# Kernel tuning notes

Measured on AMD Instinct MI355X. Metric: run time of the kernel, lower is better.

## Reference

```python
import jax, jax.numpy as jnp
import numpy as np

EPS = 1e-5
H = 8  # num_heads

def _bn(x, g, b):
    # training-mode BatchNorm over the LAST axis as channels; stats over all other axes
    axes = tuple(range(x.ndim - 1))
    mean = jnp.mean(x, axis=axes)
    var = jnp.var(x, axis=axes)  # biased, matches torch BN normalization
    return (x - mean) * jax.lax.rsqrt(var + EPS) * g + b


def setup_inputs() -> dict:
    key = jax.random.key(0)
    ks = jax.random.split(key, 16)
    m, S, C = 256, 128, 256
    s = 1.0 / np.sqrt(C)
    inp = {
        'x': jax.random.normal(ks[0], (m, S, C), jnp.float32),
        'g_n': jnp.ones((C,), jnp.float32), 'b_n': jnp.zeros((C,), jnp.float32),
        'Wq': jax.random.normal(ks[1], (C, C), jnp.float32) * s,
        'Wk': jax.random.normal(ks[2], (C, C), jnp.float32) * s,
        'Wv': jax.random.normal(ks[3], (C, C), jnp.float32) * s,
        'Wo': jax.random.normal(ks[4], (C, C), jnp.float32) * s,
        'bo': jnp.zeros((C,), jnp.float32),
        'g_pe': jnp.ones((S * S,), jnp.float32), 'b_pe': jnp.zeros((S * S,), jnp.float32),
        'g0': jnp.ones((C,), jnp.float32), 'b0': jnp.zeros((C,), jnp.float32),
        'W0': jax.random.normal(ks[5], (2 * C, C), jnp.float32) * s,
        'g1': jnp.ones((2 * C,), jnp.float32), 'b1': jnp.zeros((2 * C,), jnp.float32),
        'W1': jax.random.normal(ks[6], (C, 2 * C), jnp.float32) * (1.0 / np.sqrt(2 * C)),
    }
    return inp


def reference(x, g_n, b_n, Wq, Wk, Wv, Wo, bo, g_pe, b_pe, g0, b0, W0, g1, b1, W1):
    m, S, C = x.shape
    d = C // H
    # --- SelfAttention ---
    h = _bn(x, g_n, b_n)  # BN over channels C, stats over (batch, seq)
    q = (h @ Wq.T).reshape(m, S, H, d)
    k = (h @ Wk.T).reshape(m, S, H, d)
    v = (h @ Wv.T).reshape(m, S, H, d)
    energy = jnp.einsum('nqhc,nkhc->nhqk', q, k)  # [m,H,S,S]
    # BatchNorm1d over the flattened S*S 'channel' axis, stats over (batch, heads)
    e = energy.reshape(m, H, S * S)
    e = _bn(e, g_pe, b_pe)
    energy_post = e.reshape(m, H, S, S)
    attn = jax.nn.softmax(energy_post / jnp.sqrt(jnp.float32(C)), axis=-1)
    o = jnp.einsum('nhql,nlhc->nqhc', attn, v).reshape(m, S, C)
    x1 = o @ Wo.T + bo + x  # residual
    # --- FFN block ---
    out0 = _bn(x1, g0, b0)
    out1 = jax.nn.relu(out0)
    out2 = out1 @ W0.T            # [m,S,2C]
    out3 = _bn(out2, g1, b1)
    out4 = jax.nn.relu(out3)
    out5 = out4 @ W1.T            # [m,S,C]
    return x1 + out5  # dropout p=0.0 -> identity
```

## Files before the change

kernel.cpp:

```cpp
#include <hip/hip_runtime.h>
#include <hip/hip_bf16.h>

#define HH 8
#define SS 128
#define CC 256
#define DD 32
#define NTOK 32768
#define NHB 2048
#define BNEPS 1e-5f

using bf16 = __hip_bfloat16;
typedef float f32x4 __attribute__((ext_vector_type(4)));
typedef __bf16 bf16x8 __attribute__((ext_vector_type(8)));

__device__ __forceinline__ bf16x8 ld8(const bf16* p) {
    return *reinterpret_cast<const bf16x8*>(p);
}
__device__ __forceinline__ f32x4 ldf4(const float* p) {
    return *reinterpret_cast<const f32x4*>(p);
}
__device__ __forceinline__ void st8(bf16* p, bf16x8 v) {
    *reinterpret_cast<bf16x8*>(p) = v;
}
__device__ __forceinline__ bf16 bfc(__bf16 x) {
    union { __bf16 i; bf16 o; } u;
    u.i = x;
    return u.o;
}
__device__ __forceinline__ int swzg(int row, int g) {
    return ((g & 8) | ((g & 7) ^ (row & 7))) << 3;
}

typedef __attribute__((address_space(1))) const void g_void;
typedef __attribute__((address_space(3))) void l_void;
__device__ __forceinline__ void gload_lds16(const bf16* g, bf16* l) {
    __builtin_amdgcn_global_load_lds((g_void*)g, (l_void*)l, 16, 0, 0);
}

__global__ __launch_bounds__(256) void prep(const float* __restrict__ wq,
                                            const float* __restrict__ wk,
                                            const float* __restrict__ wv,
                                            const float* __restrict__ wo,
                                            const float* __restrict__ w0,
                                            const float* __restrict__ w1,
                                            bf16* __restrict__ out,
                                            const float* __restrict__ X,
                                            float* __restrict__ part) {
    int tid = threadIdx.x;
    if (blockIdx.x < 512) {
        int i = (blockIdx.x * 256 + tid) * 4;
        const float* src;
        int off;
        if (i < 65536) { src = wq; off = i; }
        else if (i < 131072) { src = wk; off = i - 65536; }
        else if (i < 196608) { src = wv; off = i - 131072; }
        else if (i < 262144) { src = wo; off = i - 196608; }
        else if (i < 393216) { src = w0; off = i - 262144; }
        else { src = w1; off = i - 393216; }
        f32x4 v = ldf4(src + off);
#pragma unroll
        for (int u = 0; u < 4; u++) out[i + u] = __float2bfloat16(v[u]);
        return;
    }
    int bx = blockIdx.x - 512;
    int cv = tid & 63, slot = tid >> 6;
    int c0 = cv * 4;
    size_t row0 = (size_t)bx * 256 + slot;
    float s[4], s2[4];
#pragma unroll
    for (int u = 0; u < 4; u++) { s[u] = 0.f; s2[u] = 0.f; }
    for (int i = 0; i < 64; i++) {
        size_t row = row0 + (size_t)i * 4;
        f32x4 v = ldf4(X + row * 256 + c0);
#pragma unroll
        for (int u = 0; u < 4; u++) {
            float f = v[u];
            s[u] += f; s2[u] += f * f;
        }
    }
    __shared__ float red[256][8];
#pragma unroll
    for (int u = 0; u < 4; u++) {
        red[tid][u] = s[u];
        red[tid][4 + u] = s2[u];
    }
    __syncthreads();
    if (tid < 64) {
#pragma unroll
        for (int sl = 1; sl < 4; sl++)
#pragma unroll
            for (int u = 0; u < 4; u++) {
                s[u] += red[tid + sl * 64][u];
                s2[u] += red[tid + sl * 64][4 + u];
            }
        float* dst = part + (size_t)bx * 512;
#pragma unroll
        for (int u = 0; u < 4; u++) {
            dst[c0 + u] = s[u];
            dst[256 + c0 + u] = s2[u];
        }
    }
}

template <int CH, int P, int ROWS>
__global__ __launch_bounds__(256) void statsA_wide(const bf16* __restrict__ X,
                                                   float* __restrict__ part) {
    constexpr int RB = ROWS / P;
    int c0 = (blockIdx.x * 256 + threadIdx.x) * 8;
    size_t row0 = (size_t)blockIdx.y * RB;
    float s[8], s2[8];
#pragma unroll
    for (int u = 0; u < 8; u++) { s[u] = 0.f; s2[u] = 0.f; }
    for (int i = 0; i < RB; i++) {
        bf16x8 v = ld8(X + (row0 + i) * CH + c0);
#pragma unroll
        for (int u = 0; u < 8; u++) {
            float f = (float)v[u];
            s[u] += f; s2[u] += f * f;
        }
    }
    float* dst = part + (size_t)blockIdx.y * (2 * CH);
#pragma unroll
    for (int u = 0; u < 8; u++) {
        dst[c0 + u] = s[u];
        dst[CH + c0 + u] = s2[u];
    }
}

__global__ __launch_bounds__(256) void statsB(const float* __restrict__ part, int P,
                                              int nch, float inv_n, float ps,
                                              const float* __restrict__ gamma,
                                              const float* __restrict__ beta,
                                              float* __restrict__ scale,
                                              float* __restrict__ bias) {
    int cl = threadIdx.x & 63, sl = threadIdx.x >> 6;
    int c = blockIdx.x * 64 + cl;
    float s = 0.f, s2 = 0.f;
    for (int p = sl; p < P; p += 4) {
        s += part[(size_t)p * 2 * nch + c];
        s2 += part[(size_t)p * 2 * nch + nch + c];
    }
    __shared__ float red[2][4][64];
    red[0][sl][cl] = s;
    red[1][sl][cl] = s2;
    __syncthreads();
    if (threadIdx.x < 64) {
        s = red[0][0][cl] + red[0][1][cl] + red[0][2][cl] + red[0][3][cl];
        s2 = red[1][0][cl] + red[1][1][cl] + red[1][2][cl] + red[1][3][cl];
        float mean = s * inv_n;
        float var = s2 * inv_n - mean * mean;
        float rstd = rsqrtf(var + BNEPS);
        float sc = gamma[c] * rstd;
        scale[c] = sc * ps;
        bias[c] = (beta[c] - mean * sc) * ps;
    }
}

template <bool RELU, int CH>
__global__ __launch_bounds__(256) void bn_apply_f32(const float* __restrict__ X,
                                                    bf16* __restrict__ out,
                                                    const float* __restrict__ scale,
                                                    const float* __restrict__ bias) {
    size_t base = ((size_t)blockIdx.x * 256 + threadIdx.x) * 8;
    int c0 = (int)(base & (size_t)(CH - 1));
    f32x4 x0 = ldf4(X + base), x1 = ldf4(X + base + 4);
    f32x4 s0 = ldf4(scale + c0), s1 = ldf4(scale + c0 + 4);
    f32x4 b0 = ldf4(bias + c0), b1 = ldf4(bias + c0 + 4);
    bf16x8 o;
#pragma unroll
    for (int u = 0; u < 4; u++) {
        float v = x0[u] * s0[u] + b0[u];
        if (RELU) v = fmaxf(v, 0.f);
        o[u] = (__bf16)__float2bfloat16(v);
    }
#pragma unroll
    for (int u = 0; u < 4; u++) {
        float v = x1[u] * s1[u] + b1[u];
        if (RELU) v = fmaxf(v, 0.f);
        o[u + 4] = (__bf16)__float2bfloat16(v);
    }
    st8(out + base, o);
}

template <bool RELU, int CH>
__global__ __launch_bounds__(256) void bn_apply_bf16(const bf16* __restrict__ X,
                                                     bf16* __restrict__ out,
                                                     const float* __restrict__ scale,
                                                     const float* __restrict__ bias) {
    size_t base = ((size_t)blockIdx.x * 256 + threadIdx.x) * 8;
    int c0 = (int)(base & (size_t)(CH - 1));
    bf16x8 xv = ld8(X + base);
    f32x4 s0 = ldf4(scale + c0), s1 = ldf4(scale + c0 + 4);
    f32x4 b0 = ldf4(bias + c0), b1 = ldf4(bias + c0 + 4);
    bf16x8 o;
#pragma unroll
    for (int u = 0; u < 4; u++) {
        float v = (float)xv[u] * s0[u] + b0[u];
        if (RELU) v = fmaxf(v, 0.f);
        o[u] = (__bf16)__float2bfloat16(v);
    }
#pragma unroll
    for (int u = 0; u < 4; u++) {
        float v = (float)xv[u + 4] * s1[u] + b1[u];
        if (RELU) v = fmaxf(v, 0.f);
        o[u + 4] = (__bf16)__float2bfloat16(v);
    }
    st8(out + base, o);
}

template <int MODE, bool STATS>
__device__ __forceinline__ void gemm_core(const bf16* __restrict__ A,
                                          const bf16* __restrict__ B, int m0, int n0,
                                          int N, int K, const float* __restrict__ bias,
                                          const float* __restrict__ resf,
                                          bf16* __restrict__ outb,
                                          float* __restrict__ outf,
                                          float* __restrict__ spart, char* smem) {
    bf16* As = (bf16*)smem;
    bf16* Bs = As + 128 * 64;
    int tid = threadIdx.x;
    int lane = tid & 63, wave = tid >> 6;
    int quad = lane >> 4, l16 = lane & 15;
    int wm = (wave >> 1) * 64, wn = (wave & 1) * 64;
    int srow = lane >> 3;
    int scol = (lane & 7) * 8;
    const bf16* Ab = A + (size_t)m0 * K;
    const bf16* Bb = B + (size_t)n0 * K;
    f32x4 acc[4][4];
#pragma unroll
    for (int i = 0; i < 4; i++)
#pragma unroll
        for (int j = 0; j < 4; j++) acc[i][j] = f32x4{0.f, 0.f, 0.f, 0.f};

    for (int kt = 0; kt < K; kt += 64) {
        if (kt) __syncthreads();
#pragma unroll
        for (int i = 0; i < 4; i++) {
            int r = i * 32 + wave * 8;
            gload_lds16(Ab + (size_t)(r + srow) * K + kt + scol, As + r * 64);
            gload_lds16(Bb + (size_t)(r + srow) * K + kt + scol, Bs + r * 64);
        }
        __syncthreads();
#pragma unroll
        for (int ks = 0; ks < 2; ks++) {
            int kb_ = ks * 32 + quad * 8;
            bf16x8 af[4], bfr[4];
#pragma unroll
            for (int i = 0; i < 4; i++)
                af[i] = ld8(As + (wm + i * 16 + l16) * 64 + kb_);
#pragma unroll
            for (int j = 0; j < 4; j++)
                bfr[j] = ld8(Bs + (wn + j * 16 + l16) * 64 + kb_);
#pragma unroll
            for (int i = 0; i < 4; i++)
#pragma unroll
                for (int j = 0; j < 4; j++)
                    acc[i][j] = __builtin_amdgcn_mfma_f32_16x16x32_bf16(
                        af[i], bfr[j], acc[i][j], 0, 0, 0);
        }
    }
    __syncthreads();

    if (MODE == 0) {
        bf16(*Ct)[136] = (bf16(*)[136])smem;
#pragma unroll
        for (int i = 0; i < 4; i++)
#pragma unroll
            for (int j = 0; j < 4; j++)
#pragma unroll
                for (int r = 0; r < 4; r++)
                    Ct[wm + i * 16 + quad * 4 + r][wn + j * 16 + l16] =
                        __float2bfloat16(acc[i][j][r]);
        __syncthreads();
        float s[8], s2[8];
        if (STATS) {
#pragma unroll
            for (int u = 0; u < 8; u++) { s[u] = 0.f; s2[u] = 0.f; }
        }
#pragma unroll
        for (int it = 0; it < 8; it++) {
            int idx = it * 256 + tid;
            int row = idx >> 4, colv = idx & 15;
            bf16x8 c = ld8(&Ct[row][colv * 8]);
            st8(outb + (size_t)(m0 + row) * N + n0 + colv * 8, c);
            if (STATS) {
#pragma unroll
                for (int u = 0; u < 8; u++) {
                    float f = (float)c[u];
                    s[u] += f; s2[u] += f * f;
                }
            }
        }
        if (STATS) {
            __syncthreads();
            float* rf = (float*)smem;
            int g = tid & 15, k = tid >> 4;
#pragma unroll
            for (int u = 0; u < 8; u++) {
                rf[(g * 16 + k) * 16 + u] = s[u];
                rf[(g * 16 + k) * 16 + 8 + u] = s2[u];
            }
            __syncthreads();
            if (tid < 16) {
                float a[8], b[8];
#pragma unroll
                for (int u = 0; u < 8; u++) { a[u] = 0.f; b[u] = 0.f; }
                for (int k2 = 0; k2 < 16; k2++)
#pragma unroll
                    for (int u = 0; u < 8; u++) {
                        a[u] += rf[(tid * 16 + k2) * 16 + u];
                        b[u] += rf[(tid * 16 + k2) * 16 + 8 + u];
                    }
                float* dst = spart + (size_t)(m0 >> 7) * 2 * N + n0 + tid * 8;
#pragma unroll
                for (int u = 0; u < 8; u++) {
                    dst[u] = a[u];
                    dst[N + u] = b[u];
                }
            }
        }
    } else {
        float(*Cf)[132] = (float(*)[132])smem;
        float s[4], s2[4];
        if (STATS) {
#pragma unroll
            for (int u = 0; u < 4; u++) { s[u] = 0.f; s2[u] = 0.f; }
        }
#pragma unroll
        for (int h = 0; h < 2; h++) {
            if (h) __syncthreads();
            if ((wm >> 6) == h) {
#pragma unroll
                for (int i = 0; i < 4; i++)
#pragma unroll
                    for (int j = 0; j < 4; j++)
#pragma unroll
                        for (int r = 0; r < 4; r++)
                            Cf[i * 16 + quad * 4 + r][wn + j * 16 + l16] = acc[i][j][r];
            }
            __syncthreads();
#pragma unroll
            for (int it = 0; it < 8; it++) {
                int idx = it * 256 + tid;
                int row = idx >> 5, cv = (idx & 31) * 4;
                f32x4 v = ldf4(&Cf[row][cv]);
                int gc = n0 + cv;
                size_t gi = (size_t)(m0 + h * 64 + row) * N + gc;
                f32x4 rr = ldf4(resf + gi);
                if (MODE == 1) {
                    f32x4 bb = ldf4(bias + gc);
                    v = v + bb + rr;
                } else {
                    v = v + rr;
                }
                *reinterpret_cast<f32x4*>(outf + gi) = v;
                if (STATS) {
#pragma unroll
                    for (int u = 0; u < 4; u++) {
                        s[u] += v[u]; s2[u] += v[u] * v[u];
                    }
                }
            }
        }
        if (STATS) {
            __syncthreads();
            float* rf = (float*)smem;
            int g = tid & 31, k = tid >> 5;
#pragma unroll
            for (int u = 0; u < 4; u++) {
                rf[(g * 8 + k) * 8 + u] = s[u];
                rf[(g * 8 + k) * 8 + 4 + u] = s2[u];
            }
            __syncthreads();
            if (tid < 32) {
                float a[4], b[4];
#pragma unroll
                for (int u = 0; u < 4; u++) { a[u] = 0.f; b[u] = 0.f; }
                for (int k2 = 0; k2 < 8; k2++)
#pragma unroll
                    for (int u = 0; u < 4; u++) {
                        a[u] += rf[(tid * 8 + k2) * 8 + u];
                        b[u] += rf[(tid * 8 + k2) * 8 + 4 + u];
                    }
                float* dst = spart + (size_t)(m0 >> 7) * 2 * N + n0 + tid * 4;
#pragma unroll
                for (int u = 0; u < 4; u++) {
                    dst[u] = a[u];
                    dst[N + u] = b[u];
                }
            }
        }
    }
}

template <int MODE, bool STATS>
__global__ __launch_bounds__(256) void gemm128(const bf16* __restrict__ A,
                                               const bf16* __restrict__ B, int N, int K,
                                               const float* __restrict__ bias,
                                               const float* __restrict__ resf,
                                               bf16* __restrict__ outb,
                                               float* __restrict__ outf,
                                               float* __restrict__ spart) {
    __shared__ __align__(16) char smem[34816];
    gemm_core<MODE, STATS>(A, B, blockIdx.x * 128, blockIdx.y * 128, N, K, bias, resf,
                           outb, outf, spart, smem);
}

__global__ __launch_bounds__(256) void gemm_qkv128(const bf16* __restrict__ hbuf,
                                                   const bf16* __restrict__ W,
                                                   bf16* __restrict__ qkv) {
    __shared__ __align__(16) char smem[34816];
    int mat = blockIdx.y >> 1;
    int n0 = (blockIdx.y & 1) * 128;
    gemm_core<0, false>(hbuf, W + mat * 65536, blockIdx.x * 128, n0, CC, CC, nullptr,
                        nullptr, qkv + (size_t)mat * 8388608, nullptr, nullptr, smem);
}

__global__ __launch_bounds__(256) void gemm_energy(const bf16* __restrict__ q,
                                                   const bf16* __restrict__ k,
                                                   bf16* __restrict__ E) {
    int nh = blockIdx.x;
    int nb = nh >> 3, hh = nh & 7;
    int tid = threadIdx.x;
    int lane = tid & 63, wave = tid >> 6;
    int quad = lane >> 4, l16 = lane & 15;
    int wm = (wave >> 1) * 64, wn = (wave & 1) * 64;
    size_t tb = (size_t)nb * SS;
    int cb = hh * DD + quad * 8;
    f32x4 zero = {0.f, 0.f, 0.f, 0.f};
    f32x4 acc[4][4];
#pragma unroll
    for (int i = 0; i < 4; i++)
#pragma unroll
        for (int j = 0; j < 4; j++) acc[i][j] = zero;
    bf16x8 af[4], bfg[4];
#pragma unroll
    for (int i = 0; i < 4; i++)
        af[i] = ld8(q + (tb + wm + i * 16 + l16) * CC + cb);
#pragma unroll
    for (int j = 0; j < 4; j++)
        bfg[j] = ld8(k + (tb + wn + j * 16 + l16) * CC + cb);
#pragma unroll
    for (int i = 0; i < 4; i++)
#pragma unroll
        for (int j = 0; j < 4; j++)
            acc[i][j] = __builtin_amdgcn_mfma_f32_16x16x32_bf16(af[i], bfg[j], acc[i][j], 0, 0, 0);
    __shared__ bf16 Et[128][136];
#pragma unroll
    for (int i = 0; i < 4; i++)
#pragma unroll
        for (int j = 0; j < 4; j++)
#pragma unroll
            for (int r = 0; r < 4; r++)
                Et[wm + i * 16 + quad * 4 + r][wn + j * 16 + l16] =
                    __float2bfloat16(acc[i][j][r]);
    __syncthreads();
    bf16* Eb = E + (size_t)nh * SS * SS;
#pragma unroll
    for (int it = 0; it < 8; it++) {
        int idx = it * 256 + tid;
        int row = idx >> 4, colv = idx & 15;
        st8(Eb + (size_t)row * SS + colv * 8, ld8(&Et[row][colv * 8]));
    }
}

__global__ __launch_bounds__(256, 4) void att_kernel(
    const bf16* __restrict__ E, const bf16* __restrict__ v,
    const float* __restrict__ pe_scale, const float* __restrict__ pe_bias,
    bf16* __restrict__ o) {
    __shared__ bf16 P[SS * 128];
    __shared__ bf16 Vt[DD * 128];
    int nh = blockIdx.x;
    int nb = nh >> 3, hh = nh & 7;
    const bf16* Eb = E + (size_t)nh * SS * SS;
    int tid = threadIdx.x;
    int wave = tid >> 6, lane = tid & 63;
    {
        int s = tid >> 1, d0 = (tid & 1) * 16;
        const bf16* vp = v + (size_t)(nb * SS + s) * CC + hh * DD + d0;
        bf16x8 v0 = ld8(vp), v1 = ld8(vp + 8);
        int g = s >> 3, sub = s & 7;
#pragma unroll
        for (int u = 0; u < 8; u++) {
            int da = d0 + u, db = d0 + 8 + u;
            Vt[da * 128 + swzg(da, g) + sub] = bfc(v0[u]);
            Vt[db * 128 + swzg(db, g) + sub] = bfc(v1[u]);
        }
    }
    int rs = lane >> 4, cg = lane & 15;
#pragma unroll
    for (int p = 0; p < 8; p++) {
        int r = wave * 32 + p * 4 + rs;
        int e8 = r * 128 + cg * 8;
        bf16x8 ev = ld8(Eb + e8);
        f32x4 s0 = ldf4(pe_scale + e8), s1 = ldf4(pe_scale + e8 + 4);
        f32x4 b0 = ldf4(pe_bias + e8), b1 = ldf4(pe_bias + e8 + 4);
        float l[8];
#pragma unroll
        for (int u = 0; u < 4; u++) l[u] = (float)ev[u] * s0[u] + b0[u];
#pragma unroll
        for (int u = 0; u < 4; u++) l[u + 4] = (float)ev[u + 4] * s1[u] + b1[u];
        float mx = fmaxf(fmaxf(fmaxf(l[0], l[1]), fmaxf(l[2], l[3])),
                         fmaxf(fmaxf(l[4], l[5]), fmaxf(l[6], l[7])));
#pragma unroll
        for (int off = 8; off; off >>= 1) mx = fmaxf(mx, __shfl_xor(mx, off, 16));
        float e[8], sm = 0.f;
#pragma unroll
        for (int u = 0; u < 8; u++) { e[u] = __expf(l[u] - mx); sm += e[u]; }
#pragma unroll
        for (int off = 8; off; off >>= 1) sm += __shfl_xor(sm, off, 16);
        float inv = 1.0f / sm;
        bf16x8 pv;
#pragma unroll
        for (int u = 0; u < 8; u++) pv[u] = (__bf16)__float2bfloat16(e[u] * inv);
        st8(&P[r * 128 + swzg(r, cg)], pv);
    }
    __syncthreads();
    int quad = lane >> 4, l16 = lane & 15;
    f32x4 acc[2][2];
#pragma unroll
    for (int i = 0; i < 2; i++)
#pragma unroll
        for (int j = 0; j < 2; j++) acc[i][j] = f32x4{0.f, 0.f, 0.f, 0.f};
#pragma unroll
    for (int kk = 0; kk < SS; kk += 32) {
        int g = (kk >> 3) + quad;
        int r0 = wave * 32 + l16, r1 = r0 + 16;
        bf16x8 a0 = ld8(&P[r0 * 128 + swzg(r0, g)]);
        bf16x8 a1 = ld8(&P[r1 * 128 + swzg(r1, g)]);
        bf16x8 b0 = ld8(&Vt[l16 * 128 + swzg(l16, g)]);
        bf16x8 b1 = ld8(&Vt[(l16 + 16) * 128 + swzg(l16 + 16, g)]);
        acc[0][0] = __builtin_amdgcn_mfma_f32_16x16x32_bf16(a0, b0, acc[0][0], 0, 0, 0);
        acc[0][1] = __builtin_amdgcn_mfma_f32_16x16x32_bf16(a0, b1, acc[0][1], 0, 0, 0);
        acc[1][0] = __builtin_amdgcn_mfma_f32_16x16x32_bf16(a1, b0, acc[1][0], 0, 0, 0);
        acc[1][1] = __builtin_amdgcn_mfma_f32_16x16x32_bf16(a1, b1, acc[1][1], 0, 0, 0);
    }
    __syncthreads();
    bf16* Ob = P;
#pragma unroll
    for (int i = 0; i < 2; i++)
#pragma unroll
        for (int j = 0; j < 2; j++)
#pragma unroll
            for (int r = 0; r < 4; r++) {
                int row = wave * 32 + i * 16 + quad * 4 + r;
                int col = j * 16 + l16;
                Ob[row * 40 + col] = __float2bfloat16(acc[i][j][r]);
            }
    __syncthreads();
#pragma unroll
    for (int it = 0; it < 2; it++) {
        int idx = it * 256 + tid;
        int row = idx >> 2, colv = idx & 3;
        st8(o + (size_t)(nb * SS + row) * CC + hh * DD + colv * 8,
            ld8(&Ob[row * 40 + colv * 8]));
    }
}

#define WB_OFF 0u
#define HB_OFF 1048576u
#define Q_OFF 17825792u
#define K_OFF 34603008u
#define VT_OFF 51380224u
#define E_OFF 68157440u
#define O_OFF 1048576u
#define X1_OFF 17825792u
#define OUT1_OFF 51380224u
#define OUT2_OFF 68157440u
#define OUT4_OFF 101711872u

extern "C" void kernel_launch(void* const* d_in, const int* in_sizes, int n_in,
                              void* d_out, int out_size, void* d_ws, size_t ws_size,
                              hipStream_t stream) {
    const float* x = (const float*)d_in[0];
    const float* g_n = (const float*)d_in[1];
    const float* b_n = (const float*)d_in[2];
    const float* Wq = (const float*)d_in[3];
    const float* Wk = (const float*)d_in[4];
    const float* Wv = (const float*)d_in[5];
    const float* Wo = (const float*)d_in[6];
    const float* bo = (const float*)d_in[7];
    const float* g_pe = (const float*)d_in[8];
    const float* b_pe = (const float*)d_in[9];
    const float* g0 = (const float*)d_in[10];
    const float* b0 = (const float*)d_in[11];
    const float* W0 = (const float*)d_in[12];
    const float* g1 = (const float*)d_in[13];
    const float* b1 = (const float*)d_in[14];
    const float* W1 = (const float*)d_in[15];

    char* ws = (char*)d_ws;
    bf16* WB = (bf16*)(ws + WB_OFF);
    bf16* WOB = WB + 196608;
    bf16* W0B = WB + 262144;
    bf16* W1B = WB + 393216;
    bf16* hbuf = (bf16*)(ws + HB_OFF);
    bf16* qb = (bf16*)(ws + Q_OFF);
    bf16* kb = (bf16*)(ws + K_OFF);
    bf16* vb = (bf16*)(ws + VT_OFF);
    bf16* Ebuf = (bf16*)(ws + E_OFF);
    bf16* obuf = (bf16*)(ws + O_OFF);
    float* x1 = (float*)(ws + X1_OFF);
    bf16* out1 = (bf16*)(ws + OUT1_OFF);
    bf16* out2 = (bf16*)(ws + OUT2_OFF);
    bf16* out4 = (bf16*)(ws + OUT4_OFF);
    float* bn1_scale = (float*)(ws + E_OFF);
    float* bn1_bias = bn1_scale + 256;
    float* xpart = (float*)(ws + E_OFF + 65536);
    float* pe_scale = (float*)(ws + Q_OFF);
    float* pe_bias = pe_scale + 16384;
    float* pepart = (float*)(ws + Q_OFF + 131072);
    float* bn0_scale = (float*)(ws + HB_OFF);
    float* bn0_bias = bn0_scale + 256;
    float* f1_scale = (float*)(ws + HB_OFF + 4096);
    float* f1_bias = f1_scale + 512;
    float* x1part = (float*)(ws + VT_OFF);
    float* f1part = (float*)(ws + HB_OFF + 16384);
    float* outp = (float*)d_out;

    prep<<<640, 256, 0, stream>>>(Wq, Wk, Wv, Wo, W0, W1, WB, x, xpart);
    statsB<<<4, 256, 0, stream>>>(xpart, 128, 256, 1.0f / 32768.0f, 1.0f, g_n, b_n,
                                  bn1_scale, bn1_bias);
    bn_apply_f32<false, 256><<<4096, 256, 0, stream>>>(x, hbuf, bn1_scale, bn1_bias);
    gemm_qkv128<<<dim3(256, 6), 256, 0, stream>>>(hbuf, WB, qb);
    gemm_energy<<<NHB, 256, 0, stream>>>(qb, kb, Ebuf);
    statsA_wide<16384, 32, 2048><<<dim3(8, 32), 256, 0, stream>>>(Ebuf, pepart);
    statsB<<<256, 256, 0, stream>>>(pepart, 32, 16384, 1.0f / 2048.0f, 0.0625f, g_pe,
                                    b_pe, pe_scale, pe_bias);
    att_kernel<<<NHB, 256, 0, stream>>>(Ebuf, vb, pe_scale, pe_bias, obuf);
    gemm128<1, true><<<dim3(256, 2), 256, 0, stream>>>(obuf, WOB, CC, CC, bo, x,
                                                       nullptr, x1, x1part);
    statsB<<<4, 256, 0, stream>>>(x1part, 256, 256, 1.0f / 32768.0f, 1.0f, g0, b0,
                                  bn0_scale, bn0_bias);
    bn_apply_f32<true, 256><<<4096, 256, 0, stream>>>(x1, out1, bn0_scale, bn0_bias);
    gemm128<0, true><<<dim3(256, 4), 256, 0, stream>>>(out1, W0B, 2 * CC, CC, nullptr,
                                                       nullptr, out2, nullptr, f1part);
    statsB<<<8, 256, 0, stream>>>(f1part, 256, 512, 1.0f / 32768.0f, 1.0f, g1, b1,
                                  f1_scale, f1_bias);
    bn_apply_bf16<true, 512><<<8192, 256, 0, stream>>>(out2, out4, f1_scale, f1_bias);
    gemm128<2, false><<<dim3(256, 2), 256, 0, stream>>>(out4, W1B, CC, 2 * CC, nullptr,
                                                        x1, nullptr, outp, nullptr);
    (void)in_sizes; (void)n_in; (void)out_size; (void)ws_size;
    (void)kb; (void)vb;
}
```

Baseline: 337.7 us.

## Fuse BatchNorm apply into GEMM A-operand loading

Removes the three standalone BN-apply kernels and instead applies the per-channel scale/bias (and ReLU) while loading the A tile of the following GEMM. Fp32 or bf16 activations are read directly, normalized in registers, and written to LDS. This avoids writing and re-reading intermediate bf16 buffers and cuts kernel launches. In exchange, A loads change from async global-to-LDS copies to register-path loads with extra ALU work, and each A tile is re-normalized once per N block.

```diff
diff --git a/kernel.cpp b/kernel.cpp
--- a/kernel.cpp
+++ b/kernel.cpp
@@ -156,66 +156,14 @@
     }
 }
 
-template <bool RELU, int CH>
-__global__ __launch_bounds__(256) void bn_apply_f32(const float* __restrict__ X,
-                                                    bf16* __restrict__ out,
-                                                    const float* __restrict__ scale,
-                                                    const float* __restrict__ bias) {
-    size_t base = ((size_t)blockIdx.x * 256 + threadIdx.x) * 8;
-    int c0 = (int)(base & (size_t)(CH - 1));
-    f32x4 x0 = ldf4(X + base), x1 = ldf4(X + base + 4);
-    f32x4 s0 = ldf4(scale + c0), s1 = ldf4(scale + c0 + 4);
-    f32x4 b0 = ldf4(bias + c0), b1 = ldf4(bias + c0 + 4);
-    bf16x8 o;
-#pragma unroll
-    for (int u = 0; u < 4; u++) {
-        float v = x0[u] * s0[u] + b0[u];
-        if (RELU) v = fmaxf(v, 0.f);
-        o[u] = (__bf16)__float2bfloat16(v);
-    }
-#pragma unroll
-    for (int u = 0; u < 4; u++) {
-        float v = x1[u] * s1[u] + b1[u];
-        if (RELU) v = fmaxf(v, 0.f);
-        o[u + 4] = (__bf16)__float2bfloat16(v);
-    }
-    st8(out + base, o);
-}
-
-template <bool RELU, int CH>
-__global__ __launch_bounds__(256) void bn_apply_bf16(const bf16* __restrict__ X,
-                                                     bf16* __restrict__ out,
-                                                     const float* __restrict__ scale,
-                                                     const float* __restrict__ bias) {
-    size_t base = ((size_t)blockIdx.x * 256 + threadIdx.x) * 8;
-    int c0 = (int)(base & (size_t)(CH - 1));
-    bf16x8 xv = ld8(X + base);
-    f32x4 s0 = ldf4(scale + c0), s1 = ldf4(scale + c0 + 4);
-    f32x4 b0 = ldf4(bias + c0), b1 = ldf4(bias + c0 + 4);
-    bf16x8 o;
-#pragma unroll
-    for (int u = 0; u < 4; u++) {
-        float v = (float)xv[u] * s0[u] + b0[u];
-        if (RELU) v = fmaxf(v, 0.f);
-        o[u] = (__bf16)__float2bfloat16(v);
-    }
-#pragma unroll
-    for (int u = 0; u < 4; u++) {
-        float v = (float)xv[u + 4] * s1[u] + b1[u];
-        if (RELU) v = fmaxf(v, 0.f);
-        o[u + 4] = (__bf16)__float2bfloat16(v);
-    }
-    st8(out + base, o);
-}
-
-template <int MODE, bool STATS>
-__device__ __forceinline__ void gemm_core(const bf16* __restrict__ A,
-                                          const bf16* __restrict__ B, int m0, int n0,
-                                          int N, int K, const float* __restrict__ bias,
-                                          const float* __restrict__ resf,
-                                          bf16* __restrict__ outb,
-                                          float* __restrict__ outf,
-                                          float* __restrict__ spart, char* smem) {
+template <int MODE, bool STATS, int ASRC>
+__device__ __forceinline__ void gemm_core(
+    const bf16* __restrict__ A, const float* __restrict__ Af,
+    const bf16* __restrict__ B, int m0, int n0, int N, int K,
+    const float* __restrict__ a_scale, const float* __restrict__ a_bias,
+    const float* __restrict__ bias, const float* __restrict__ resf,
+    bf16* __restrict__ outb, float* __restrict__ outf, float* __restrict__ spart,
+    char* smem) {
     bf16* As = (bf16*)smem;
     bf16* Bs = As + 128 * 64;
     int tid = threadIdx.x;
@@ -224,7 +172,7 @@
     int wm = (wave >> 1) * 64, wn = (wave & 1) * 64;
     int srow = lane >> 3;
     int scol = (lane & 7) * 8;
-    const bf16* Ab = A + (size_t)m0 * K;
+    const bf16* Ab = (ASRC == 0) ? A + (size_t)m0 * K : A;
     const bf16* Bb = B + (size_t)n0 * K;
     f32x4 acc[4][4];
 #pragma unroll
@@ -237,8 +185,54 @@
 #pragma unroll
         for (int i = 0; i < 4; i++) {
             int r = i * 32 + wave * 8;
-            gload_lds16(Ab + (size_t)(r + srow) * K + kt + scol, As + r * 64);
             gload_lds16(Bb + (size_t)(r + srow) * K + kt + scol, Bs + r * 64);
+        }
+        if (ASRC == 0) {
+#pragma unroll
+            for (int i = 0; i < 4; i++) {
+                int r = i * 32 + wave * 8;
+                gload_lds16(Ab + (size_t)(r + srow) * K + kt + scol, As + r * 64);
+            }
+        } else {
+            int c = kt + scol;
+            f32x4 s0 = ldf4(a_scale + c), s1 = ldf4(a_scale + c + 4);
+            f32x4 b0 = ldf4(a_bias + c), b1 = ldf4(a_bias + c + 4);
+#pragma unroll
+            for (int i = 0; i < 4; i++) {
+                int r = i * 32 + wave * 8;
+                size_t row = (size_t)(m0 + r + srow);
+                bf16x8 av;
+                if (ASRC == 3) {
+                    bf16x8 xv = ld8(Ab + row * K + c);
+#pragma unroll
+                    for (int u = 0; u < 4; u++) {
+                        float f = (float)xv[u] * s0[u] + b0[u];
+                        f = fmaxf(f, 0.f);
+                        av[u] = (__bf16)__float2bfloat16(f);
+                    }
+#pragma unroll
+                    for (int u = 0; u < 4; u++) {
+                        float f = (float)xv[u + 4] * s1[u] + b1[u];
+                        f = fmaxf(f, 0.f);
+                        av[u + 4] = (__bf16)__float2bfloat16(f);
+                    }
+                } else {
+                    f32x4 x0 = ldf4(Af + row * K + c), x1v = ldf4(Af + row * K + c + 4);
+#pragma unroll
+                    for (int u = 0; u < 4; u++) {
+                        float f = x0[u] * s0[u] + b0[u];
+                        if (ASRC == 2) f = fmaxf(f, 0.f);
+                        av[u] = (__bf16)__float2bfloat16(f);
+                    }
+#pragma unroll
+                    for (int u = 0; u < 4; u++) {
+                        float f = x1v[u] * s1[u] + b1[u];
+                        if (ASRC == 2) f = fmaxf(f, 0.f);
+                        av[u + 4] = (__bf16)__float2bfloat16(f);
+                    }
+                }
+                st8(As + r * 64 + lane * 8, av);
+            }
         }
         __syncthreads();
 #pragma unroll
@@ -393,27 +387,29 @@
     }
 }
 
-template <int MODE, bool STATS>
-__global__ __launch_bounds__(256) void gemm128(const bf16* __restrict__ A,
-                                               const bf16* __restrict__ B, int N, int K,
-                                               const float* __restrict__ bias,
-                                               const float* __restrict__ resf,
-                                               bf16* __restrict__ outb,
-                                               float* __restrict__ outf,
-                                               float* __restrict__ spart) {
+template <int MODE, bool STATS, int ASRC>
+__global__ __launch_bounds__(256) void gemm128(
+    const bf16* __restrict__ A, const float* __restrict__ Af,
+    const bf16* __restrict__ B, int N, int K, const float* __restrict__ a_scale,
+    const float* __restrict__ a_bias, const float* __restrict__ bias,
+    const float* __restrict__ resf, bf16* __restrict__ outb,
+    float* __restrict__ outf, float* __restrict__ spart) {
     __shared__ __align__(16) char smem[34816];
-    gemm_core<MODE, STATS>(A, B, blockIdx.x * 128, blockIdx.y * 128, N, K, bias, resf,
-                           outb, outf, spart, smem);
-}
-
-__global__ __launch_bounds__(256) void gemm_qkv128(const bf16* __restrict__ hbuf,
+    gemm_core<MODE, STATS, ASRC>(A, Af, B, blockIdx.x * 128, blockIdx.y * 128, N, K,
+                                 a_scale, a_bias, bias, resf, outb, outf, spart, smem);
+}
+
+__global__ __launch_bounds__(256) void gemm_qkv128(const float* __restrict__ x,
                                                    const bf16* __restrict__ W,
+                                                   const float* __restrict__ a_scale,
+                                                   const float* __restrict__ a_bias,
                                                    bf16* __restrict__ qkv) {
     __shared__ __align__(16) char smem[34816];
     int mat = blockIdx.y >> 1;
     int n0 = (blockIdx.y & 1) * 128;
-    gemm_core<0, false>(hbuf, W + mat * 65536, blockIdx.x * 128, n0, CC, CC, nullptr,
-                        nullptr, qkv + (size_t)mat * 8388608, nullptr, nullptr, smem);
+    gemm_core<0, false, 1>(nullptr, x, W + mat * 65536, blockIdx.x * 128, n0, CC, CC,
+                           a_scale, a_bias, nullptr, nullptr,
+                           qkv + (size_t)mat * 8388608, nullptr, nullptr, smem);
 }
 
 __global__ __launch_bounds__(256) void gemm_energy(const bf16* __restrict__ q,
@@ -558,16 +554,13 @@
 }
 
 #define WB_OFF 0u
-#define HB_OFF 1048576u
+#define O_OFF 1048576u
 #define Q_OFF 17825792u
 #define K_OFF 34603008u
 #define VT_OFF 51380224u
 #define E_OFF 68157440u
-#define O_OFF 1048576u
 #define X1_OFF 17825792u
-#define OUT1_OFF 51380224u
 #define OUT2_OFF 68157440u
-#define OUT4_OFF 101711872u
 
 extern "C" void kernel_launch(void* const* d_in, const int* in_sizes, int n_in,
                               void* d_out, int out_size, void* d_ws, size_t ws_size,
@@ -594,52 +587,48 @@
     bf16* WOB = WB + 196608;
     bf16* W0B = WB + 262144;
     bf16* W1B = WB + 393216;
-    bf16* hbuf = (bf16*)(ws + HB_OFF);
     bf16* qb = (bf16*)(ws + Q_OFF);
     bf16* kb = (bf16*)(ws + K_OFF);
     bf16* vb = (bf16*)(ws + VT_OFF);
     bf16* Ebuf = (bf16*)(ws + E_OFF);
     bf16* obuf = (bf16*)(ws + O_OFF);
     float* x1 = (float*)(ws + X1_OFF);
-    bf16* out1 = (bf16*)(ws + OUT1_OFF);
     bf16* out2 = (bf16*)(ws + OUT2_OFF);
-    bf16* out4 = (bf16*)(ws + OUT4_OFF);
     float* bn1_scale = (float*)(ws + E_OFF);
     float* bn1_bias = bn1_scale + 256;
     float* xpart = (float*)(ws + E_OFF + 65536);
     float* pe_scale = (float*)(ws + Q_OFF);
     float* pe_bias = pe_scale + 16384;
     float* pepart = (float*)(ws + Q_OFF + 131072);
-    float* bn0_scale = (float*)(ws + HB_OFF);
+    float* bn0_scale = (float*)(ws + O_OFF);
     float* bn0_bias = bn0_scale + 256;
-    float* f1_scale = (float*)(ws + HB_OFF + 4096);
+    float* f1_scale = (float*)(ws + O_OFF + 4096);
     float* f1_bias = f1_scale + 512;
     float* x1part = (float*)(ws + VT_OFF);
-    float* f1part = (float*)(ws + HB_OFF + 16384);
+    float* f1part = (float*)(ws + O_OFF + 16384);
     float* outp = (float*)d_out;
 
     prep<<<640, 256, 0, stream>>>(Wq, Wk, Wv, Wo, W0, W1, WB, x, xpart);
     statsB<<<4, 256, 0, stream>>>(xpart, 128, 256, 1.0f / 32768.0f, 1.0f, g_n, b_n,
                                   bn1_scale, bn1_bias);
-    bn_apply_f32<false, 256><<<4096, 256, 0, stream>>>(x, hbuf, bn1_scale, bn1_bias);
-    gemm_qkv128<<<dim3(256, 6), 256, 0, stream>>>(hbuf, WB, qb);
+    gemm_qkv128<<<dim3(256, 6), 256, 0, stream>>>(x, WB, bn1_scale, bn1_bias, qb);
     gemm_energy<<<NHB, 256, 0, stream>>>(qb, kb, Ebuf);
     statsA_wide<16384, 32, 2048><<<dim3(8, 32), 256, 0, stream>>>(Ebuf, pepart);
     statsB<<<256, 256, 0, stream>>>(pepart, 32, 16384, 1.0f / 2048.0f, 0.0625f, g_pe,
                                     b_pe, pe_scale, pe_bias);
     att_kernel<<<NHB, 256, 0, stream>>>(Ebuf, vb, pe_scale, pe_bias, obuf);
-    gemm128<1, true><<<dim3(256, 2), 256, 0, stream>>>(obuf, WOB, CC, CC, bo, x,
-                                                       nullptr, x1, x1part);
+    gemm128<1, true, 0><<<dim3(256, 2), 256, 0, stream>>>(
+        obuf, nullptr, WOB, CC, CC, nullptr, nullptr, bo, x, nullptr, x1, x1part);
     statsB<<<4, 256, 0, stream>>>(x1part, 256, 256, 1.0f / 32768.0f, 1.0f, g0, b0,
                                   bn0_scale, bn0_bias);
-    bn_apply_f32<true, 256><<<4096, 256, 0, stream>>>(x1, out1, bn0_scale, bn0_bias);
-    gemm128<0, true><<<dim3(256, 4), 256, 0, stream>>>(out1, W0B, 2 * CC, CC, nullptr,
-                                                       nullptr, out2, nullptr, f1part);
+    gemm128<0, true, 2><<<dim3(256, 4), 256, 0, stream>>>(
+        nullptr, x1, W0B, 2 * CC, CC, bn0_scale, bn0_bias, nullptr, nullptr, out2,
+        nullptr, f1part);
     statsB<<<8, 256, 0, stream>>>(f1part, 256, 512, 1.0f / 32768.0f, 1.0f, g1, b1,
                                   f1_scale, f1_bias);
-    bn_apply_bf16<true, 512><<<8192, 256, 0, stream>>>(out2, out4, f1_scale, f1_bias);
-    gemm128<2, false><<<dim3(256, 2), 256, 0, stream>>>(out4, W1B, CC, 2 * CC, nullptr,
-                                                        x1, nullptr, outp, nullptr);
+    gemm128<2, false, 3><<<dim3(256, 2), 256, 0, stream>>>(
+        out2, nullptr, W1B, CC, 2 * CC, f1_scale, f1_bias, nullptr, x1, nullptr, outp,
+        nullptr);
     (void)in_sizes; (void)n_in; (void)out_size; (void)ws_size;
     (void)kb; (void)vb;
 }
```

New measurement: 328.6 us. 2.7% less time.
